# Kernel optimization log

Hardware: AMD Instinct MI355X
Metric: run time of the kernel (lower is better)

The kernel has to match this reference:

```python
import jax, jax.numpy as jnp
import numpy as np

LOG_PROB_FACTOR = 0.5  # logProbFactor


def setup_inputs() -> dict:
    key = jax.random.key(0)
    ks = jax.random.split(key, 8)
    B, L, F, K = 2048, 512, 64, 2
    s = jax.random.randint(ks[0], (B, L), 0, K)
    W0 = jax.random.normal(ks[1], (K, F), jnp.float32) / np.sqrt(K).astype(np.float32)
    b0 = jnp.zeros((F,), jnp.float32)
    # fused LSTM weights, gate order (i, f, g, o); flax: dense_i no bias, dense_h has bias
    Wi = jax.random.normal(ks[2], (F, 4 * F), jnp.float32) / np.sqrt(F).astype(np.float32)
    Wh = jax.random.normal(ks[3], (F, 4 * F), jnp.float32) / np.sqrt(F).astype(np.float32)
    bh = jnp.zeros((4 * F,), jnp.float32)
    Wa = jax.random.normal(ks[4], (F, K), jnp.float32) / np.sqrt(F).astype(np.float32)
    ba = jnp.zeros((K,), jnp.float32)
    Wp = jax.random.normal(ks[5], (F, 1), jnp.float32) / np.sqrt(F).astype(np.float32)
    bp = jnp.zeros((1,), jnp.float32)
    return {"s": s, "W0": W0, "b0": b0, "Wi": Wi, "Wh": Wh, "bh": bh,
            "Wa": Wa, "ba": ba, "Wp": Wp, "bp": bp}


def _forward(s, W0, b0, Wi, Wh, bh, Wa, ba, Wp, bp):
    B, L = s.shape
    K, F = W0.shape
    # pad a leading zero token: input at step t is spin at site t-1
    s_pad = jnp.pad(s, ((0, 0), (1, 0)))                       # [B, L+1]
    x = jax.nn.one_hot(s_pad, K, dtype=W0.dtype) @ W0 + b0     # layer0: [B, L+1, F]
    xs = jnp.swapaxes(x, 0, 1)                                 # [L+1, B, F] time-major
    c0 = jnp.zeros((B, F), x.dtype)
    h0 = jnp.zeros((B, F), x.dtype)

    def step(carry, xt):
        c, h = carry
        g = xt @ Wi + h @ Wh + bh                              # [B, 4F]
        i, f, gg, o = jnp.split(g, 4, axis=-1)
        cn = jax.nn.sigmoid(f) * c + jax.nn.sigmoid(i) * jnp.tanh(gg)
        hn = jax.nn.sigmoid(o) * jnp.tanh(cn)
        return (cn, hn), hn

    _, ys = jax.lax.scan(step, (c0, h0), xs)                   # [L+1, B, F]

    logits = ys[:-1] @ Wa + ba                                 # [L, B, K]
    logp = jax.nn.log_softmax(logits, axis=-1) * LOG_PROB_FACTOR
    picked = jnp.take_along_axis(logp, s.T[..., None], axis=-1)[..., 0]  # [L, B]
    amp = picked.sum(axis=0)                                   # [B]
    phase = (ys[-1] @ Wp + bp)[..., 0]                         # [B]
    return amp + 1j * phase                                    # complex log-psi per sample


def reference(s, W0, b0, Wi, Wh, bh, Wa, ba, Wp, bp):
    return _forward(s, W0, b0, Wi, Wh, bh, Wa, ba, Wp, bp)
```

## Files before the change

### kernel.cpp

```cpp
#include <hip/hip_runtime.h>
#include <math.h>

typedef _Float16 f16x8 __attribute__((ext_vector_type(8)));
typedef float    f32x4 __attribute__((ext_vector_type(4)));
typedef _Float16 f16x2 __attribute__((ext_vector_type(2)));
typedef __fp16   fp16x2 __attribute__((ext_vector_type(2)));

#define B_TOT 2048
#define LSEQ  512
#define NS    8
#define LOG2E 1.44269504088896f
#define LN2   0.69314718055995f

#define MFMA16(A, B, C) __builtin_amdgcn_mfma_f32_16x16x32_f16((A), (B), (C), 0, 0, 0)

__device__ __forceinline__ unsigned int pkrtz(float a, float b) {
    fp16x2 p = __builtin_amdgcn_cvt_pkrtz(a, b);
    return __builtin_bit_cast(unsigned int, p);
}

__global__ __launch_bounds__(256, 1)
void lstm_v16_kernel(const int* __restrict__ s,
                     const float* __restrict__ W0, const float* __restrict__ b0,
                     const float* __restrict__ Wi, const float* __restrict__ Wh,
                     const float* __restrict__ bh, const float* __restrict__ Wa,
                     const float* __restrict__ ba, const float* __restrict__ Wp,
                     const float* __restrict__ bp, float* __restrict__ out)
{
    const int tid  = threadIdx.x;
    const int w    = tid >> 6;
    const int lane = tid & 63;
    const int n    = lane & 15;
    const int q    = lane >> 4;
    const int ns   = n & 7;
    const int hi   = n >> 3;
    const int b0s  = blockIdx.x * NS;

    __shared__ __align__(16) unsigned int HhD[2][512];
    __shared__ unsigned short TOKB[LSEQ + 2];
    __shared__ unsigned char  SRAW[NS][LSEQ];
    __shared__ _Float16 DBUF[LSEQ][NS];
    __shared__ float PART[32][NS];

    for (int i = tid; i < NS * LSEQ; i += 256)
        SRAW[i >> 9][i & 511] = (unsigned char)s[(b0s + (i >> 9)) * LSEQ + (i & 511)];
    __syncthreads();
    for (int u = tid; u <= LSEQ; u += 256) {
        unsigned int mask = 0;
        if (u >= 1) {
            #pragma unroll
            for (int m = 0; m < NS; ++m)
                mask |= ((unsigned int)SRAW[m][u - 1]) << m;
        }
        TOKB[u] = (unsigned short)mask;
    }

    f16x8 awh[4][2];
    #pragma unroll
    for (int g = 0; g < 4; ++g) {
        const float sc  = (g == 2) ? (2.0f * LOG2E) : (-LOG2E);
        const int   col = 64 * g + 16 * w + n;
        #pragma unroll
        for (int c = 0; c < 2; ++c)
            #pragma unroll
            for (int j = 0; j < 8; ++j)
                awh[g][c][j] = (_Float16)(Wh[(32 * c + 8 * q + j) * 256 + col] * sc);
    }

    f16x8 awd[2];
    #pragma unroll
    for (int c = 0; c < 2; ++c)
        #pragma unroll
        for (int j = 0; j < 8; ++j) {
            int k = 32 * c + 8 * q + j;
            awd[c][j] = (_Float16)((n == 0) ? (Wa[2 * k + 1] - Wa[2 * k]) : 0.0f);
        }
    const float dba = ba[1] - ba[0];

    f32x4 p0q[4], dpq[4];
    {
        float a0[4][4], a1[4][4];
        #pragma unroll
        for (int g = 0; g < 4; ++g)
            #pragma unroll
            for (int r = 0; r < 4; ++r) {
                float bb = bh[64 * g + 16 * w + 4 * q + r];
                a0[g][r] = bb; a1[g][r] = bb;
            }
        for (int f = 0; f < 64; ++f) {
            float wb0 = W0[f]      + b0[f];
            float wb1 = W0[64 + f] + b0[f];
            #pragma unroll
            for (int g = 0; g < 4; ++g) {
                const float4 wi4 = *(const float4*)&Wi[f * 256 + 64 * g + 16 * w + 4 * q];
                #pragma unroll
                for (int r = 0; r < 4; ++r) {
                    float wi = (&wi4.x)[r];
                    a0[g][r] = fmaf(wb0, wi, a0[g][r]);
                    a1[g][r] = fmaf(wb1, wi, a1[g][r]);
                }
            }
        }
        #pragma unroll
        for (int g = 0; g < 4; ++g) {
            const float sc = (g == 2) ? (2.0f * LOG2E) : (-LOG2E);
            #pragma unroll
            for (int r = 0; r < 4; ++r) {
                p0q[g][r] = a0[g][r] * sc;
                dpq[g][r] = (a1[g][r] - a0[g][r]) * sc;
            }
        }
    }

    __syncthreads();

    const int wAddr = 4 * ns + 64 * (q >> 1) + 128 * w + 2 * (q & 1) + hi;
    const int rAddr = 4 * ns + 64 * (q & 1) + 128 * (q >> 1);

    float h2[2] = {0, 0}, c2[2] = {0, 0};
    f32x4 ci[4];
    #pragma unroll
    for (int g = 0; g < 4; ++g) ci[g] = p0q[g];

    float dpend = 0.0f;
    int   tpend = -1;

    #pragma unroll 4
    for (int v = 0; v <= LSEQ; ++v) {
        const int p = v & 1;
        unsigned int* __restrict__ hb = &HhD[p][0];

        hb[wAddr] = pkrtz(h2[0], h2[1]);
        __syncthreads();

        if (tpend >= 0) {
            if (lane < 8) DBUF[tpend][lane] = (_Float16)dpend;
            tpend = -1;
        }

        uint4 r0 = *(const uint4*)&hb[rAddr];
        uint4 r1 = *(const uint4*)&hb[rAddr + 256];
        const f16x8 bf0 = __builtin_bit_cast(f16x8, r0);
        const f16x8 bf1 = __builtin_bit_cast(f16x8, r1);

        const unsigned int tokm_next = (v < LSEQ) ? (unsigned int)TOKB[v + 1] : 0u;

        f32x4 acc0 = ci[0], acc1 = ci[1], acc2 = ci[2], acc3 = ci[3];
        acc0 = MFMA16(awh[0][0], bf0, acc0);
        acc1 = MFMA16(awh[1][0], bf0, acc1);
        acc2 = MFMA16(awh[2][0], bf0, acc2);
        acc3 = MFMA16(awh[3][0], bf0, acc3);
        acc0 = MFMA16(awh[0][1], bf1, acc0);
        acc1 = MFMA16(awh[1][1], bf1, acc1);
        acc2 = MFMA16(awh[2][1], bf1, acc2);
        acc3 = MFMA16(awh[3][1], bf1, acc3);

        if (v >= 1 && w == (v & 3)) {
            f32x4 da = (f32x4){dba, dba, dba, dba};
            da = MFMA16(awd[0], bf0, da);
            da = MFMA16(awd[1], bf1, da);
            dpend = da[0];
            tpend = v - 1;
        }

        const float sel = (float)((tokm_next >> ns) & 1u);
        const f32x4 sel4 = {sel, sel, sel, sel};
        #pragma unroll
        for (int g = 0; g < 4; ++g)
            ci[g] = dpq[g] * sel4 + p0q[g];

        const bool hb2 = (hi != 0);
        float gi[2] = { hb2 ? acc0[2] : acc0[0], hb2 ? acc0[3] : acc0[1] };
        float gf[2] = { hb2 ? acc1[2] : acc1[0], hb2 ? acc1[3] : acc1[1] };
        float gg[2] = { hb2 ? acc2[2] : acc2[0], hb2 ? acc2[3] : acc2[1] };
        float go[2] = { hb2 ? acc3[2] : acc3[0], hb2 ? acc3[3] : acc3[1] };

        #pragma unroll
        for (int rr = 0; rr < 2; ++rr) {
            float ei = __builtin_amdgcn_exp2f(gi[rr]);
            float ef = __builtin_amdgcn_exp2f(gf[rr]);
            float eg = __builtin_amdgcn_exp2f(gg[rr]);
            float eo = __builtin_amdgcn_exp2f(go[rr]);
            float P  = (1.0f + ei) * (eg + 1.0f);
            float F  = 1.0f + ef;
            float R2 = __builtin_amdgcn_rcpf(P * F);
            float cn = fmaf(c2[rr] * P, R2, (eg - 1.0f) * F * R2);
            c2[rr] = cn;
            float ec = __builtin_amdgcn_exp2f(fminf(cn * (2.0f * LOG2E), 60.f));
            float Ro = __builtin_amdgcn_rcpf((1.0f + eo) * (ec + 1.0f));
            h2[rr] = (ec - 1.0f) * Ro;
        }
    }

    if (tpend >= 0 && lane < 8) DBUF[tpend][lane] = (_Float16)dpend;
    HhD[1][wAddr] = pkrtz(h2[0], h2[1]);
    __syncthreads();

    {
        const int nn = tid & 7;
        const int cp = tid >> 3;
        float a = 0.0f;
        #pragma unroll 4
        for (int k = 0; k < 16; ++k) {
            int t = cp * 16 + k;
            float d = (float)DBUF[t][nn];
            float x = SRAW[nn][t] ? -d : d;
            float e = __builtin_amdgcn_exp2f(-fabsf(x) * LOG2E);
            a += fmaxf(x, 0.0f) + __builtin_amdgcn_logf(1.0f + e) * LN2;
        }
        PART[cp][nn] = a;
    }
    __syncthreads();

    if (tid < 8) {
        float ssum = 0.0f;
        #pragma unroll
        for (int c = 0; c < 32; ++c) ssum += PART[c][tid];
        out[b0s + tid] = -0.5f * ssum;
    }

    if (w == 0) {
        float ph = 0.0f;
        #pragma unroll
        for (int d = 0; d < 4; ++d) {
            unsigned int ua = HhD[1][4 * ns + 128 * q + d];
            unsigned int ub = HhD[1][4 * ns + 64 + 128 * q + d];
            f16x2 ha  = __builtin_bit_cast(f16x2, ua);
            f16x2 hc  = __builtin_bit_cast(f16x2, ub);
            ph = fmaf((float)ha[0], Wp[16 * q + 2 * d],
                 fmaf((float)ha[1], Wp[16 * q + 2 * d + 1], ph));
            ph = fmaf((float)hc[0], Wp[16 * q + 8 + 2 * d],
                 fmaf((float)hc[1], Wp[16 * q + 8 + 2 * d + 1], ph));
        }
        ph += __shfl_xor(ph, 16, 64);
        ph += __shfl_xor(ph, 32, 64);
        if (q == 0 && n < 8) out[B_TOT + b0s + n] = ph + bp[0];
    }
}

extern "C" void kernel_launch(void* const* d_in, const int* in_sizes, int n_in,
                              void* d_out, int out_size, void* d_ws, size_t ws_size,
                              hipStream_t stream) {
    const int*   s  = (const int*)  d_in[0];
    const float* W0 = (const float*)d_in[1];
    const float* b0 = (const float*)d_in[2];
    const float* Wi = (const float*)d_in[3];
    const float* Wh = (const float*)d_in[4];
    const float* bh = (const float*)d_in[5];
    const float* Wa = (const float*)d_in[6];
    const float* ba = (const float*)d_in[7];
    const float* Wp = (const float*)d_in[8];
    const float* bp = (const float*)d_in[9];
    float* out = (float*)d_out;

    dim3 grid(B_TOT / NS);
    dim3 block(256);
    lstm_v16_kernel<<<grid, block, 0, stream>>>(s, W0, b0, Wi, Wh, bh,
                                                Wa, ba, Wp, bp, out);
}
```

Baseline: 277.1 us.

## Halve samples per block to four and run two blocks per CU

Each block now handles 4 batch samples instead of 8, which doubles the grid to 512 blocks. Each lane now owns one hidden unit of one sample instead of two, so the per-step activation work per lane is halved. Launch bounds move to 2 blocks per CU so two independent recurrences can interleave and hide the per-step barrier and MFMA latency. The cost is that the MFMA N dimension of 16 is now only partly used by real samples, so matrix work per sample doubles, and the h-buffer layout and final reductions change to match.

```diff
diff --git a/kernel.cpp b/kernel.cpp
--- a/kernel.cpp
+++ b/kernel.cpp
@@ -8,19 +8,14 @@
 
 #define B_TOT 2048
 #define LSEQ  512
-#define NS    8
+#define NS    4
 #define LOG2E 1.44269504088896f
 #define LN2   0.69314718055995f
 
 #define MFMA16(A, B, C) __builtin_amdgcn_mfma_f32_16x16x32_f16((A), (B), (C), 0, 0, 0)
 
-__device__ __forceinline__ unsigned int pkrtz(float a, float b) {
-    fp16x2 p = __builtin_amdgcn_cvt_pkrtz(a, b);
-    return __builtin_bit_cast(unsigned int, p);
-}
-
-__global__ __launch_bounds__(256, 1)
-void lstm_v16_kernel(const int* __restrict__ s,
+__global__ __launch_bounds__(256, 2)
+void lstm_v18_kernel(const int* __restrict__ s,
                      const float* __restrict__ W0, const float* __restrict__ b0,
                      const float* __restrict__ Wi, const float* __restrict__ Wh,
                      const float* __restrict__ bh, const float* __restrict__ Wa,
@@ -32,15 +27,15 @@
     const int lane = tid & 63;
     const int n    = lane & 15;
     const int q    = lane >> 4;
-    const int ns   = n & 7;
-    const int hi   = n >> 3;
+    const int ns   = n & 3;
+    const int cp   = n >> 2;
     const int b0s  = blockIdx.x * NS;
 
-    __shared__ __align__(16) unsigned int HhD[2][512];
-    __shared__ unsigned short TOKB[LSEQ + 2];
+    __shared__ __align__(16) unsigned int HhD[2][128];
+    __shared__ unsigned char  TOKW[LSEQ + 2];
     __shared__ unsigned char  SRAW[NS][LSEQ];
     __shared__ _Float16 DBUF[LSEQ][NS];
-    __shared__ float PART[32][NS];
+    __shared__ float PART[64][NS];
 
     for (int i = tid; i < NS * LSEQ; i += 256)
         SRAW[i >> 9][i & 511] = (unsigned char)s[(b0s + (i >> 9)) * LSEQ + (i & 511)];
@@ -52,7 +47,7 @@
             for (int m = 0; m < NS; ++m)
                 mask |= ((unsigned int)SRAW[m][u - 1]) << m;
         }
-        TOKB[u] = (unsigned short)mask;
+        TOKW[u] = (unsigned char)mask;
     }
 
     f16x8 awh[4][2];
@@ -114,10 +109,10 @@
 
     __syncthreads();
 
-    const int wAddr = 4 * ns + 64 * (q >> 1) + 128 * w + 2 * (q & 1) + hi;
-    const int rAddr = 4 * ns + 64 * (q & 1) + 128 * (q >> 1);
-
-    float h2[2] = {0, 0}, c2[2] = {0, 0};
+    const int wIdx = 64 * ns + 16 * w + 4 * q + cp;
+    const int rAddr = 32 * ns + 4 * q;
+
+    float h1 = 0.f, c1 = 0.f;
     f32x4 ci[4];
     #pragma unroll
     for (int g = 0; g < 4; ++g) ci[g] = p0q[g];
@@ -130,20 +125,20 @@
         const int p = v & 1;
         unsigned int* __restrict__ hb = &HhD[p][0];
 
-        hb[wAddr] = pkrtz(h2[0], h2[1]);
+        ((_Float16*)hb)[wIdx] = (_Float16)h1;
         __syncthreads();
 
         if (tpend >= 0) {
-            if (lane < 8) DBUF[tpend][lane] = (_Float16)dpend;
+            if (lane < NS) DBUF[tpend][lane] = (_Float16)dpend;
             tpend = -1;
         }
 
         uint4 r0 = *(const uint4*)&hb[rAddr];
-        uint4 r1 = *(const uint4*)&hb[rAddr + 256];
+        uint4 r1 = *(const uint4*)&hb[rAddr + 16];
         const f16x8 bf0 = __builtin_bit_cast(f16x8, r0);
         const f16x8 bf1 = __builtin_bit_cast(f16x8, r1);
 
-        const unsigned int tokm_next = (v < LSEQ) ? (unsigned int)TOKB[v + 1] : 0u;
+        const unsigned int tokm_next = (v < LSEQ) ? (unsigned int)TOKW[v + 1] : 0u;
 
         f32x4 acc0 = ci[0], acc1 = ci[1], acc2 = ci[2], acc3 = ci[3];
         acc0 = MFMA16(awh[0][0], bf0, acc0);
@@ -169,72 +164,70 @@
         for (int g = 0; g < 4; ++g)
             ci[g] = dpq[g] * sel4 + p0q[g];
 
-        const bool hb2 = (hi != 0);
-        float gi[2] = { hb2 ? acc0[2] : acc0[0], hb2 ? acc0[3] : acc0[1] };
-        float gf[2] = { hb2 ? acc1[2] : acc1[0], hb2 ? acc1[3] : acc1[1] };
-        float gg[2] = { hb2 ? acc2[2] : acc2[0], hb2 ? acc2[3] : acc2[1] };
-        float go[2] = { hb2 ? acc3[2] : acc3[0], hb2 ? acc3[3] : acc3[1] };
-
-        #pragma unroll
-        for (int rr = 0; rr < 2; ++rr) {
-            float ei = __builtin_amdgcn_exp2f(gi[rr]);
-            float ef = __builtin_amdgcn_exp2f(gf[rr]);
-            float eg = __builtin_amdgcn_exp2f(gg[rr]);
-            float eo = __builtin_amdgcn_exp2f(go[rr]);
+        const bool s1 = (cp & 1) != 0;
+        const bool s2 = (cp & 2) != 0;
+        float gi = s2 ? (s1 ? acc0[3] : acc0[2]) : (s1 ? acc0[1] : acc0[0]);
+        float gf = s2 ? (s1 ? acc1[3] : acc1[2]) : (s1 ? acc1[1] : acc1[0]);
+        float gg = s2 ? (s1 ? acc2[3] : acc2[2]) : (s1 ? acc2[1] : acc2[0]);
+        float go = s2 ? (s1 ? acc3[3] : acc3[2]) : (s1 ? acc3[1] : acc3[0]);
+
+        {
+            float ei = __builtin_amdgcn_exp2f(gi);
+            float ef = __builtin_amdgcn_exp2f(gf);
+            float eg = __builtin_amdgcn_exp2f(gg);
+            float eo = __builtin_amdgcn_exp2f(go);
             float P  = (1.0f + ei) * (eg + 1.0f);
             float F  = 1.0f + ef;
             float R2 = __builtin_amdgcn_rcpf(P * F);
-            float cn = fmaf(c2[rr] * P, R2, (eg - 1.0f) * F * R2);
-            c2[rr] = cn;
+            float cn = fmaf(c1 * P, R2, (eg - 1.0f) * F * R2);
+            c1 = cn;
             float ec = __builtin_amdgcn_exp2f(fminf(cn * (2.0f * LOG2E), 60.f));
             float Ro = __builtin_amdgcn_rcpf((1.0f + eo) * (ec + 1.0f));
-            h2[rr] = (ec - 1.0f) * Ro;
-        }
-    }
-
-    if (tpend >= 0 && lane < 8) DBUF[tpend][lane] = (_Float16)dpend;
-    HhD[1][wAddr] = pkrtz(h2[0], h2[1]);
+            h1 = (ec - 1.0f) * Ro;
+        }
+    }
+
+    if (tpend >= 0 && lane < NS) DBUF[tpend][lane] = (_Float16)dpend;
+    ((_Float16*)&HhD[1][0])[wIdx] = (_Float16)h1;
     __syncthreads();
 
     {
-        const int nn = tid & 7;
-        const int cp = tid >> 3;
+        const int nn = tid & 3;
+        const int cc = tid >> 2;
         float a = 0.0f;
         #pragma unroll 4
-        for (int k = 0; k < 16; ++k) {
-            int t = cp * 16 + k;
+        for (int k = 0; k < 8; ++k) {
+            int t = cc * 8 + k;
             float d = (float)DBUF[t][nn];
             float x = SRAW[nn][t] ? -d : d;
             float e = __builtin_amdgcn_exp2f(-fabsf(x) * LOG2E);
             a += fmaxf(x, 0.0f) + __builtin_amdgcn_logf(1.0f + e) * LN2;
         }
-        PART[cp][nn] = a;
-    }
-    __syncthreads();
-
-    if (tid < 8) {
+        PART[cc][nn] = a;
+    }
+    __syncthreads();
+
+    if (tid < NS) {
         float ssum = 0.0f;
         #pragma unroll
-        for (int c = 0; c < 32; ++c) ssum += PART[c][tid];
+        for (int c = 0; c < 64; ++c) ssum += PART[c][tid];
         out[b0s + tid] = -0.5f * ssum;
     }
 
     if (w == 0) {
-        float ph = 0.0f;
-        #pragma unroll
-        for (int d = 0; d < 4; ++d) {
-            unsigned int ua = HhD[1][4 * ns + 128 * q + d];
-            unsigned int ub = HhD[1][4 * ns + 64 + 128 * q + d];
-            f16x2 ha  = __builtin_bit_cast(f16x2, ua);
-            f16x2 hc  = __builtin_bit_cast(f16x2, ub);
-            ph = fmaf((float)ha[0], Wp[16 * q + 2 * d],
-                 fmaf((float)ha[1], Wp[16 * q + 2 * d + 1], ph));
-            ph = fmaf((float)hc[0], Wp[16 * q + 8 + 2 * d],
-                 fmaf((float)hc[1], Wp[16 * q + 8 + 2 * d + 1], ph));
-        }
-        ph += __shfl_xor(ph, 16, 64);
-        ph += __shfl_xor(ph, 32, 64);
-        if (q == 0 && n < 8) out[B_TOT + b0s + n] = ph + bp[0];
+        unsigned int ua = HhD[1][32 * q + 2 * n];
+        unsigned int ub = HhD[1][32 * q + 2 * n + 1];
+        f16x2 ha = __builtin_bit_cast(f16x2, ua);
+        f16x2 hc = __builtin_bit_cast(f16x2, ub);
+        float ph = fmaf((float)ha[0], Wp[4 * n],
+                   fmaf((float)ha[1], Wp[4 * n + 1],
+                   fmaf((float)hc[0], Wp[4 * n + 2],
+                        (float)hc[1] * Wp[4 * n + 3])));
+        ph += __shfl_xor(ph, 1, 64);
+        ph += __shfl_xor(ph, 2, 64);
+        ph += __shfl_xor(ph, 4, 64);
+        ph += __shfl_xor(ph, 8, 64);
+        if (n == 0) out[B_TOT + b0s + q] = ph + bp[0];
     }
 }
 
@@ -255,6 +248,6 @@
 
     dim3 grid(B_TOT / NS);
     dim3 block(256);
-    lstm_v16_kernel<<<grid, block, 0, stream>>>(s, W0, b0, Wi, Wh, bh,
+    lstm_v18_kernel<<<grid, block, 0, stream>>>(s, W0, b0, Wi, Wh, bh,
                                                 Wa, ba, Wp, bp, out);
 }
```

Result: slower. 303.7 us (+9.6%).
